# Kernel tuning notes

Measured on AMD Instinct MI355X. Metric: run time of the kernel, lower is better.

Reference implementation:

```python
import jax, jax.numpy as jnp
import numpy as np

G, N, D, K, OUT = 2048, 64, 128, 128, 10  # K*D == input_dim == 16384

def setup_inputs() -> dict:
    key = jax.random.key(0)
    k1, k2, k3, k4, k5 = jax.random.split(key, 5)
    x = jax.random.normal(k1, (G, N, D), dtype=jnp.float32)
    # nn.Linear(node_dim, input_dim/node_dim): weight [K, D], bias [K]
    W_att = jax.random.normal(k2, (K, D), dtype=jnp.float32) * (1.0 / np.sqrt(D))
    b_att = jax.random.normal(k3, (K,), dtype=jnp.float32) * 0.01
    # nn.Linear(input_dim, output_dim): weight [OUT, K*D], bias [OUT]
    W1 = jax.random.normal(k4, (OUT, K * D), dtype=jnp.float32) * (1.0 / np.sqrt(K * D))
    b1 = jax.random.normal(k5, (OUT,), dtype=jnp.float32) * 0.01
    return {"x": x, "W_att": W_att, "b_att": b_att, "W1": W1, "b1": b1}

def reference(x, W_att, b_att, W1, b1):
    # Per-graph gram matrix X^T X : [G, D, D], quantized to 2 decimals
    gram = jnp.einsum('gnd,gne->gde', x, x)
    gram = jnp.round(gram * 100.0) / 100.0
    # attend: Linear(D -> K) applied row-wise to gram -> attn_coef [G, D, K]
    attn = jnp.einsum('gde,ke->gdk', gram, W_att) + b_att
    # attn_weights = attn^T ([G, K, D]); pooled = attn_weights @ gram -> [G, K, D]
    pooled = jnp.einsum('gdk,gde->gke', attn, gram)
    flat = pooled.reshape(x.shape[0], K * D)  # view(input_dim)
    # linear1 (dropout omitted: eval mode)
    return flat @ W1.T + b1
```

## Files before the change

### kernel.cpp

```cpp
#include <hip/hip_runtime.h>

typedef __attribute__((ext_vector_type(8)))  __bf16 bf16x8;
typedef __attribute__((ext_vector_type(4)))  __bf16 bf16x4;
typedef __attribute__((ext_vector_type(16))) float  f32x16;

constexpr int NG  = 2048;
constexpr int NN  = 64;
constexpr int DD  = 128;
constexpr int KK  = 128;
constexpr int OUTD = 10;

__device__ __host__ inline void tileOf(int t, int& ti, int& tj) {
    if (t < 4)      { ti = 0; tj = t;     }
    else if (t < 7) { ti = 1; tj = t - 3; }
    else if (t < 9) { ti = 2; tj = t - 5; }
    else            { ti = 3; tj = 3;     }
}

__device__ inline int xtIdx(int r, int c) { return r * 64  + (c ^ ((r & 7) << 3)); }
__device__ inline int gIdx (int r, int c) { return r * 128 + (c ^ ((r & 15) << 3)); }

__global__ __launch_bounds__(128)
void precompute_kernel(const float* __restrict__ Wa,
                       const float* __restrict__ b_att,
                       const float* __restrict__ W1,
                       float* __restrict__ A,
                       float* __restrict__ c)
{
    const int o = blockIdx.x >> 7;
    const int f = blockIdx.x & 127;
    const int e = threadIdx.x;
    const float* __restrict__ W1o = W1 + (size_t)o * (KK * DD);

    float acc = 0.f, cacc = 0.f;
    for (int k = 0; k < KK; ++k) {
        const float w1 = W1o[k * DD + e];
        acc  += Wa[k * DD + f] * w1;
        cacc += b_att[k] * w1;
    }
    A[((size_t)o * DD + f) * DD + e] = acc;
    if (f == 0) c[o * DD + e] = cacc;
}

__global__ __launch_bounds__(256)
void pack_kernel(const float* __restrict__ A, __bf16* __restrict__ Sp)
{
    const int b = blockIdx.x;
    const int o = b / 10, t = b - o * 10;
    int ti, tj; tileOf(t, ti, tj);
    const int l  = threadIdx.x & 63;
    const int rq = threadIdx.x >> 6;
    const int e  = tj * 32 + (l & 31);
    const float* __restrict__ Ao = A + (size_t)o * DD * DD;

    bf16x4 p;
#pragma unroll
    for (int j = 0; j < 4; ++j) {
        const int f = ti * 32 + j + 8 * rq + 4 * (l >> 5);
        float v;
        if (f < e)       v = Ao[f * DD + e] + Ao[e * DD + f];
        else if (f == e) v = Ao[f * DD + f];
        else             v = 0.f;
        p[j] = (__bf16)v;
    }
    *(bf16x4*)&Sp[(size_t)((o * 10 + t) * 64 + l) * 16 + rq * 4] = p;
}

__device__ __forceinline__ void process_graph(
    const float* __restrict__ xg,
    __bf16* __restrict__ XtL, __bf16* __restrict__ GL,
    float (*__restrict__ sp)[DD], float* __restrict__ sOut,
    int tid, int w, int l, int l31, int l5, int extraBase,
    f32x16& hacc0, f32x16& haccX)
{
    {
        const int f = tid & 127, half = tid >> 7;
#pragma unroll
        for (int ch = 0; ch < 2; ++ch) {
            float v[8];
#pragma unroll
            for (int i = 0; i < 8; ++i) v[i] = xg[(half * 16 + ch * 8 + i) * DD + f];
            bf16x8 p;
#pragma unroll
            for (int i = 0; i < 8; ++i) p[i] = (__bf16)v[i];
            *(bf16x8*)&XtL[xtIdx(f, half * 16 + ch * 8)] = p;
        }
    }
    __syncthreads();

    const int ti  = w & 3;
    const int tj0 = (w >> 2) * 2;
    f32x16 acc0, acc1;
#pragma unroll
    for (int i = 0; i < 16; ++i) { acc0[i] = 0.f; acc1[i] = 0.f; }
    {
        const int arow  = ti  * 32 + l31;
        const int brow0 = tj0 * 32 + l31;
#pragma unroll
        for (int ks = 0; ks < 4; ++ks) {
            const int kc = ks * 16 + l5 * 8;
            bf16x8 a  = *(const bf16x8*)&XtL[xtIdx(arow, kc)];
            bf16x8 b0 = *(const bf16x8*)&XtL[xtIdx(brow0, kc)];
            bf16x8 b1 = *(const bf16x8*)&XtL[xtIdx(brow0 + 32, kc)];
            acc0 = __builtin_amdgcn_mfma_f32_32x32x16_bf16(a, b0, acc0, 0, 0, 0);
            acc1 = __builtin_amdgcn_mfma_f32_32x32x16_bf16(a, b1, acc1, 0, 0, 0);
        }
    }
    __syncthreads();

    {
        float sum0 = 0.f, sum1 = 0.f;
#pragma unroll
        for (int tt = 0; tt < 2; ++tt) {
            const int e = (tj0 + tt) * 32 + l31;
#pragma unroll
            for (int g2 = 0; g2 < 4; ++g2) {
                bf16x4 p;
#pragma unroll
                for (int j = 0; j < 4; ++j) {
                    const float av = tt ? acc1[g2 * 4 + j] : acc0[g2 * 4 + j];
                    const float q = rintf(av * 100.f) * 0.01f;
                    p[j] = (__bf16)q;
                    if (tt) sum1 += q; else sum0 += q;
                }
                const int fbase = ti * 32 + g2 * 8 + l5 * 4;
                *(bf16x4*)&GL[gIdx(e, fbase)] = p;
            }
        }
        sp[ti * 2 + l5][tj0 * 32 + l31]       = sum0;
        sp[ti * 2 + l5][(tj0 + 1) * 32 + l31] = sum1;
    }
    __syncthreads();

    if (w == 2 || w == 3) {
        const int e = (w - 2) * 64 + l;
        float s = 0.f;
#pragma unroll
        for (int i = 0; i < 8; ++i) s += sp[i][e];
        sOut[e] = s;
    }

#pragma unroll
    for (int i = 0; i < 16; ++i) hacc0[i] = 0.f;
    {
        int hti, htj; tileOf(w, hti, htj);
        const int ra = hti * 32 + l31, rb = htj * 32 + l31;
#pragma unroll
        for (int ks = 0; ks < 8; ++ks) {
            const int kc = ks * 16 + l5 * 8;
            bf16x8 a = *(const bf16x8*)&GL[gIdx(ra, kc)];
            bf16x8 b = *(const bf16x8*)&GL[gIdx(rb, kc)];
            hacc0 = __builtin_amdgcn_mfma_f32_32x32x16_bf16(a, b, hacc0, 0, 0, 0);
        }
    }
    if (w == extraBase || w == extraBase + 1) {
        int ti1, tj1; tileOf(8 + (w - extraBase), ti1, tj1);
        const int ra = ti1 * 32 + l31, rb = tj1 * 32 + l31;
#pragma unroll
        for (int ks = 0; ks < 8; ++ks) {
            const int kc = ks * 16 + l5 * 8;
            bf16x8 a = *(const bf16x8*)&GL[gIdx(ra, kc)];
            bf16x8 b = *(const bf16x8*)&GL[gIdx(rb, kc)];
            haccX = __builtin_amdgcn_mfma_f32_32x32x16_bf16(a, b, haccX, 0, 0, 0);
        }
    }
    __syncthreads();
}

__global__ __launch_bounds__(512)
void graph_kernel(const float* __restrict__ x,
                  const __bf16* __restrict__ Sp,
                  const float* __restrict__ cg,
                  const float* __restrict__ bias1,
                  float* __restrict__ out)
{
    __shared__ __align__(16) char ldsraw[20 * 512 * 4];
    __shared__ float sp[8][DD];
    __shared__ float sA[DD], sB[DD];

    __bf16* const XtL = (__bf16*)ldsraw;
    __bf16* const GL  = (__bf16*)ldsraw;
    float*  const PP  = (float*)ldsraw;

    const int g0  = blockIdx.x * 2;
    const int g1  = g0 + 1;
    const int tid = threadIdx.x;
    const int w   = tid >> 6;
    const int l   = tid & 63;
    const int l31 = l & 31;
    const int l5  = l >> 5;

    f32x16 hA0, hB0, hX1;
#pragma unroll
    for (int i = 0; i < 16; ++i) hX1[i] = 0.f;

    process_graph(x + (size_t)g0 * NN * DD, XtL, GL, sp, sA,
                  tid, w, l, l31, l5, 6, hA0, hX1);
    process_graph(x + (size_t)g1 * NN * DD, XtL, GL, sp, sB,
                  tid, w, l, l31, l5, 4, hB0, hX1);

#pragma unroll
    for (int o = 0; o < OUTD; ++o) {
        const __bf16* __restrict__ spp = Sp + (size_t)((o * 10 + w) * 64 + l) * 16;
        const bf16x8 s0 = *(const bf16x8*)&spp[0];
        const bf16x8 s1 = *(const bf16x8*)&spp[8];
        float tA = 0.f, tB = 0.f;
#pragma unroll
        for (int j = 0; j < 8; ++j) {
            const float v = (float)s0[j];
            tA += v * hA0[j];
            tB += v * hB0[j];
        }
#pragma unroll
        for (int j = 0; j < 8; ++j) {
            const float v = (float)s1[j];
            tA += v * hA0[8 + j];
            tB += v * hB0[8 + j];
        }
        if (w >= 4) {
            const __bf16* __restrict__ sp2 =
                Sp + (size_t)((o * 10 + 8 + (w & 1)) * 64 + l) * 16;
            const bf16x8 e0 = *(const bf16x8*)&sp2[0];
            const bf16x8 e1 = *(const bf16x8*)&sp2[8];
            float tx = 0.f;
#pragma unroll
            for (int j = 0; j < 8; ++j) tx += (float)e0[j] * hX1[j];
#pragma unroll
            for (int j = 0; j < 8; ++j) tx += (float)e1[j] * hX1[8 + j];
            if (w >= 6) tA += tx; else tB += tx;
        }
        if (w == 0) {
            tA += cg[o * DD + l] * sA[l] + cg[o * DD + 64 + l] * sA[64 + l];
            tB += cg[o * DD + l] * sB[l] + cg[o * DD + 64 + l] * sB[64 + l];
        }
        PP[o * 512 + tid]        = tA;
        PP[(10 + o) * 512 + tid] = tB;
    }
    __syncthreads();

    for (int p = w; p < 2 * OUTD; p += 8) {
        const float4 q0 = *(const float4*)&PP[p * 512 + l * 8];
        const float4 q1 = *(const float4*)&PP[p * 512 + l * 8 + 4];
        float v = (q0.x + q0.y) + (q0.z + q0.w) + (q1.x + q1.y) + (q1.z + q1.w);
        v += __shfl_down(v, 32, 64);
        v += __shfl_down(v, 16, 64);
        v += __shfl_down(v, 8, 64);
        v += __shfl_down(v, 4, 64);
        v += __shfl_down(v, 2, 64);
        v += __shfl_down(v, 1, 64);
        if (l == 0) {
            const int gg = (p < OUTD) ? g0 : g1;
            const int oo = (p < OUTD) ? p : p - OUTD;
            out[(size_t)gg * OUTD + oo] = v + bias1[oo];
        }
    }
}

extern "C" void kernel_launch(void* const* d_in, const int* in_sizes, int n_in,
                              void* d_out, int out_size, void* d_ws, size_t ws_size,
                              hipStream_t stream)
{
    const float* x     = (const float*)d_in[0];
    const float* Wa    = (const float*)d_in[1];
    const float* b_att = (const float*)d_in[2];
    const float* W1    = (const float*)d_in[3];
    const float* bias1 = (const float*)d_in[4];
    float* out = (float*)d_out;

    float*  A  = (float*)d_ws;
    float*  c  = A + (size_t)OUTD * DD * DD;
    __bf16* Sp = (__bf16*)(c + OUTD * DD);

    precompute_kernel<<<OUTD * DD, 128, 0, stream>>>(Wa, b_att, W1, A, c);
    pack_kernel<<<100, 256, 0, stream>>>(A, Sp);
    graph_kernel<<<NG / 2, 512, 0, stream>>>(x, Sp, c, bias1, out);
}
```

Measured before the change: 51.30 us.

## Prefetch second graph's input during first graph's gram MFMA phase

Before the first graph's gram MFMA loop, the kernel now issues the global loads for the second graph. After that loop it converts them to bf16 and stores them into a new dedicated LDS buffer, so the second graph's load latency overlaps with the first graph's compute. The first graph's staging moves into the kernel body, and the second graph's separate staging phase and its barrier are removed. The cost is 16 extra live float registers and an extra 16 KB of LDS, which may reduce occupancy.

```diff
diff --git a/kernel.cpp b/kernel.cpp
--- a/kernel.cpp
+++ b/kernel.cpp
@@ -66,27 +66,22 @@
     *(bf16x4*)&Sp[(size_t)((o * 10 + t) * 64 + l) * 16 + rq * 4] = p;
 }
 
-__device__ __forceinline__ void process_graph(
-    const float* __restrict__ xg,
-    __bf16* __restrict__ XtL, __bf16* __restrict__ GL,
+template<bool PREP_B>
+__device__ __forceinline__ void phases123(
+    const float* __restrict__ xgB,
+    const __bf16* __restrict__ XtS,
+    __bf16* __restrict__ XtLB,
+    __bf16* __restrict__ GL,
     float (*__restrict__ sp)[DD], float* __restrict__ sOut,
     int tid, int w, int l, int l31, int l5, int extraBase,
     f32x16& hacc0, f32x16& haccX)
 {
-    {
+    float vB[16];
+    if (PREP_B) {
         const int f = tid & 127, half = tid >> 7;
 #pragma unroll
-        for (int ch = 0; ch < 2; ++ch) {
-            float v[8];
-#pragma unroll
-            for (int i = 0; i < 8; ++i) v[i] = xg[(half * 16 + ch * 8 + i) * DD + f];
-            bf16x8 p;
-#pragma unroll
-            for (int i = 0; i < 8; ++i) p[i] = (__bf16)v[i];
-            *(bf16x8*)&XtL[xtIdx(f, half * 16 + ch * 8)] = p;
-        }
-    }
-    __syncthreads();
+        for (int i = 0; i < 16; ++i) vB[i] = xgB[(half * 16 + i) * DD + f];
+    }
 
     const int ti  = w & 3;
     const int tj0 = (w >> 2) * 2;
@@ -99,12 +94,21 @@
 #pragma unroll
         for (int ks = 0; ks < 4; ++ks) {
             const int kc = ks * 16 + l5 * 8;
-            bf16x8 a  = *(const bf16x8*)&XtL[xtIdx(arow, kc)];
-            bf16x8 b0 = *(const bf16x8*)&XtL[xtIdx(brow0, kc)];
-            bf16x8 b1 = *(const bf16x8*)&XtL[xtIdx(brow0 + 32, kc)];
+            bf16x8 a  = *(const bf16x8*)&XtS[xtIdx(arow, kc)];
+            bf16x8 b0 = *(const bf16x8*)&XtS[xtIdx(brow0, kc)];
+            bf16x8 b1 = *(const bf16x8*)&XtS[xtIdx(brow0 + 32, kc)];
             acc0 = __builtin_amdgcn_mfma_f32_32x32x16_bf16(a, b0, acc0, 0, 0, 0);
             acc1 = __builtin_amdgcn_mfma_f32_32x32x16_bf16(a, b1, acc1, 0, 0, 0);
         }
+    }
+
+    if (PREP_B) {
+        const int f = tid & 127, half = tid >> 7;
+        bf16x8 p0, p1;
+#pragma unroll
+        for (int i = 0; i < 8; ++i) { p0[i] = (__bf16)vB[i]; p1[i] = (__bf16)vB[8 + i]; }
+        *(bf16x8*)&XtLB[xtIdx(f, half * 16)]     = p0;
+        *(bf16x8*)&XtLB[xtIdx(f, half * 16 + 8)] = p1;
     }
     __syncthreads();
 
@@ -175,12 +179,13 @@
                   float* __restrict__ out)
 {
     __shared__ __align__(16) char ldsraw[20 * 512 * 4];
+    __shared__ __align__(16) __bf16 XtLB[DD * NN];
     __shared__ float sp[8][DD];
     __shared__ float sA[DD], sB[DD];
 
-    __bf16* const XtL = (__bf16*)ldsraw;
-    __bf16* const GL  = (__bf16*)ldsraw;
-    float*  const PP  = (float*)ldsraw;
+    __bf16* const XtLA = (__bf16*)ldsraw;
+    __bf16* const GL   = (__bf16*)ldsraw;
+    float*  const PP   = (float*)ldsraw;
 
     const int g0  = blockIdx.x * 2;
     const int g1  = g0 + 1;
@@ -189,15 +194,32 @@
     const int l   = tid & 63;
     const int l31 = l & 31;
     const int l5  = l >> 5;
+    const float* __restrict__ xgA = x + (size_t)g0 * NN * DD;
+    const float* __restrict__ xgB = x + (size_t)g1 * NN * DD;
+
+    {
+        const int f = tid & 127, half = tid >> 7;
+#pragma unroll
+        for (int ch = 0; ch < 2; ++ch) {
+            float v[8];
+#pragma unroll
+            for (int i = 0; i < 8; ++i) v[i] = xgA[(half * 16 + ch * 8 + i) * DD + f];
+            bf16x8 p;
+#pragma unroll
+            for (int i = 0; i < 8; ++i) p[i] = (__bf16)v[i];
+            *(bf16x8*)&XtLA[xtIdx(f, half * 16 + ch * 8)] = p;
+        }
+    }
+    __syncthreads();
 
     f32x16 hA0, hB0, hX1;
 #pragma unroll
     for (int i = 0; i < 16; ++i) hX1[i] = 0.f;
 
-    process_graph(x + (size_t)g0 * NN * DD, XtL, GL, sp, sA,
-                  tid, w, l, l31, l5, 6, hA0, hX1);
-    process_graph(x + (size_t)g1 * NN * DD, XtL, GL, sp, sB,
-                  tid, w, l, l31, l5, 4, hB0, hX1);
+    phases123<true>(xgB, XtLA, XtLB, GL, sp, sA,
+                    tid, w, l, l31, l5, 6, hA0, hX1);
+    phases123<false>(nullptr, XtLB, nullptr, GL, sp, sB,
+                     tid, w, l, l31, l5, 4, hB0, hX1);
 
 #pragma unroll
     for (int o = 0; o < OUTD; ++o) {
```

After: 51.83 us. No clear change (+1.0%).

## Split LDS into separate Xt and gram buffers and prefetch second graph's input

Applied to the files above, without the earlier changes.

Inlines the two per-graph passes and gives the transposed-input and gram tiles separate LDS regions, so the second graph's x is loaded into registers and written to LDS while the first graph's gram-gram MFMAs run. This removes one barrier per graph and hides global load latency behind compute. It also sets launch bounds to request two blocks per CU, and batches the final projection loop two outputs at a time with the cg values hoisted. The risks are higher register pressure from holding 16 prefetched floats plus the accumulators, and a larger LDS footprint (48 KB) that may limit occupancy.

```diff
diff --git a/kernel.cpp b/kernel.cpp
--- a/kernel.cpp
+++ b/kernel.cpp
@@ -66,121 +66,20 @@
     *(bf16x4*)&Sp[(size_t)((o * 10 + t) * 64 + l) * 16 + rq * 4] = p;
 }
 
-__device__ __forceinline__ void process_graph(
-    const float* __restrict__ xg,
-    __bf16* __restrict__ XtL, __bf16* __restrict__ GL,
-    float (*__restrict__ sp)[DD], float* __restrict__ sOut,
-    int tid, int w, int l, int l31, int l5, int extraBase,
-    f32x16& hacc0, f32x16& haccX)
-{
-    {
-        const int f = tid & 127, half = tid >> 7;
-#pragma unroll
-        for (int ch = 0; ch < 2; ++ch) {
-            float v[8];
-#pragma unroll
-            for (int i = 0; i < 8; ++i) v[i] = xg[(half * 16 + ch * 8 + i) * DD + f];
-            bf16x8 p;
-#pragma unroll
-            for (int i = 0; i < 8; ++i) p[i] = (__bf16)v[i];
-            *(bf16x8*)&XtL[xtIdx(f, half * 16 + ch * 8)] = p;
-        }
-    }
-    __syncthreads();
-
-    const int ti  = w & 3;
-    const int tj0 = (w >> 2) * 2;
-    f32x16 acc0, acc1;
-#pragma unroll
-    for (int i = 0; i < 16; ++i) { acc0[i] = 0.f; acc1[i] = 0.f; }
-    {
-        const int arow  = ti  * 32 + l31;
-        const int brow0 = tj0 * 32 + l31;
-#pragma unroll
-        for (int ks = 0; ks < 4; ++ks) {
-            const int kc = ks * 16 + l5 * 8;
-            bf16x8 a  = *(const bf16x8*)&XtL[xtIdx(arow, kc)];
-            bf16x8 b0 = *(const bf16x8*)&XtL[xtIdx(brow0, kc)];
-            bf16x8 b1 = *(const bf16x8*)&XtL[xtIdx(brow0 + 32, kc)];
-            acc0 = __builtin_amdgcn_mfma_f32_32x32x16_bf16(a, b0, acc0, 0, 0, 0);
-            acc1 = __builtin_amdgcn_mfma_f32_32x32x16_bf16(a, b1, acc1, 0, 0, 0);
-        }
-    }
-    __syncthreads();
-
-    {
-        float sum0 = 0.f, sum1 = 0.f;
-#pragma unroll
-        for (int tt = 0; tt < 2; ++tt) {
-            const int e = (tj0 + tt) * 32 + l31;
-#pragma unroll
-            for (int g2 = 0; g2 < 4; ++g2) {
-                bf16x4 p;
-#pragma unroll
-                for (int j = 0; j < 4; ++j) {
-                    const float av = tt ? acc1[g2 * 4 + j] : acc0[g2 * 4 + j];
-                    const float q = rintf(av * 100.f) * 0.01f;
-                    p[j] = (__bf16)q;
-                    if (tt) sum1 += q; else sum0 += q;
-                }
-                const int fbase = ti * 32 + g2 * 8 + l5 * 4;
-                *(bf16x4*)&GL[gIdx(e, fbase)] = p;
-            }
-        }
-        sp[ti * 2 + l5][tj0 * 32 + l31]       = sum0;
-        sp[ti * 2 + l5][(tj0 + 1) * 32 + l31] = sum1;
-    }
-    __syncthreads();
-
-    if (w == 2 || w == 3) {
-        const int e = (w - 2) * 64 + l;
-        float s = 0.f;
-#pragma unroll
-        for (int i = 0; i < 8; ++i) s += sp[i][e];
-        sOut[e] = s;
-    }
-
-#pragma unroll
-    for (int i = 0; i < 16; ++i) hacc0[i] = 0.f;
-    {
-        int hti, htj; tileOf(w, hti, htj);
-        const int ra = hti * 32 + l31, rb = htj * 32 + l31;
-#pragma unroll
-        for (int ks = 0; ks < 8; ++ks) {
-            const int kc = ks * 16 + l5 * 8;
-            bf16x8 a = *(const bf16x8*)&GL[gIdx(ra, kc)];
-            bf16x8 b = *(const bf16x8*)&GL[gIdx(rb, kc)];
-            hacc0 = __builtin_amdgcn_mfma_f32_32x32x16_bf16(a, b, hacc0, 0, 0, 0);
-        }
-    }
-    if (w == extraBase || w == extraBase + 1) {
-        int ti1, tj1; tileOf(8 + (w - extraBase), ti1, tj1);
-        const int ra = ti1 * 32 + l31, rb = tj1 * 32 + l31;
-#pragma unroll
-        for (int ks = 0; ks < 8; ++ks) {
-            const int kc = ks * 16 + l5 * 8;
-            bf16x8 a = *(const bf16x8*)&GL[gIdx(ra, kc)];
-            bf16x8 b = *(const bf16x8*)&GL[gIdx(rb, kc)];
-            haccX = __builtin_amdgcn_mfma_f32_32x32x16_bf16(a, b, haccX, 0, 0, 0);
-        }
-    }
-    __syncthreads();
-}
-
-__global__ __launch_bounds__(512)
+__global__ __launch_bounds__(512, 2)
 void graph_kernel(const float* __restrict__ x,
                   const __bf16* __restrict__ Sp,
                   const float* __restrict__ cg,
                   const float* __restrict__ bias1,
                   float* __restrict__ out)
 {
-    __shared__ __align__(16) char ldsraw[20 * 512 * 4];
+    __shared__ __align__(16) char lds48[48 * 1024];
     __shared__ float sp[8][DD];
     __shared__ float sA[DD], sB[DD];
 
-    __bf16* const XtL = (__bf16*)ldsraw;
-    __bf16* const GL  = (__bf16*)ldsraw;
-    float*  const PP  = (float*)ldsraw;
+    __bf16* const XtL = (__bf16*)lds48;
+    __bf16* const GL  = (__bf16*)(lds48 + 16 * 1024);
+    float*  const PP  = (float*)lds48;
 
     const int g0  = blockIdx.x * 2;
     const int g1  = g0 + 1;
@@ -189,52 +88,253 @@
     const int l   = tid & 63;
     const int l31 = l & 31;
     const int l5  = l >> 5;
+    const int f   = tid & 127, half = tid >> 7;
+    const float* __restrict__ xgA = x + (size_t)g0 * NN * DD;
+    const float* __restrict__ xgB = x + (size_t)g1 * NN * DD;
+
+    const int ti  = w & 3;
+    const int tj0 = (w >> 2) * 2;
+
+    {
+#pragma unroll
+        for (int ch = 0; ch < 2; ++ch) {
+            float v[8];
+#pragma unroll
+            for (int i = 0; i < 8; ++i) v[i] = xgA[(half * 16 + ch * 8 + i) * DD + f];
+            bf16x8 p;
+#pragma unroll
+            for (int i = 0; i < 8; ++i) p[i] = (__bf16)v[i];
+            *(bf16x8*)&XtL[xtIdx(f, half * 16 + ch * 8)] = p;
+        }
+    }
+    __syncthreads();
 
     f32x16 hA0, hB0, hX1;
 #pragma unroll
     for (int i = 0; i < 16; ++i) hX1[i] = 0.f;
 
-    process_graph(x + (size_t)g0 * NN * DD, XtL, GL, sp, sA,
-                  tid, w, l, l31, l5, 6, hA0, hX1);
-    process_graph(x + (size_t)g1 * NN * DD, XtL, GL, sp, sB,
-                  tid, w, l, l31, l5, 4, hB0, hX1);
-
-#pragma unroll
-    for (int o = 0; o < OUTD; ++o) {
-        const __bf16* __restrict__ spp = Sp + (size_t)((o * 10 + w) * 64 + l) * 16;
-        const bf16x8 s0 = *(const bf16x8*)&spp[0];
-        const bf16x8 s1 = *(const bf16x8*)&spp[8];
-        float tA = 0.f, tB = 0.f;
-#pragma unroll
-        for (int j = 0; j < 8; ++j) {
-            const float v = (float)s0[j];
-            tA += v * hA0[j];
-            tB += v * hB0[j];
-        }
-#pragma unroll
-        for (int j = 0; j < 8; ++j) {
-            const float v = (float)s1[j];
-            tA += v * hA0[8 + j];
-            tB += v * hB0[8 + j];
-        }
-        if (w >= 4) {
-            const __bf16* __restrict__ sp2 =
-                Sp + (size_t)((o * 10 + 8 + (w & 1)) * 64 + l) * 16;
-            const bf16x8 e0 = *(const bf16x8*)&sp2[0];
-            const bf16x8 e1 = *(const bf16x8*)&sp2[8];
-            float tx = 0.f;
-#pragma unroll
-            for (int j = 0; j < 8; ++j) tx += (float)e0[j] * hX1[j];
-#pragma unroll
-            for (int j = 0; j < 8; ++j) tx += (float)e1[j] * hX1[8 + j];
-            if (w >= 6) tA += tx; else tB += tx;
-        }
+    f32x16 acc0, acc1;
+#pragma unroll
+    for (int i = 0; i < 16; ++i) { acc0[i] = 0.f; acc1[i] = 0.f; }
+    {
+        const int arow  = ti  * 32 + l31;
+        const int brow0 = tj0 * 32 + l31;
+#pragma unroll
+        for (int ks = 0; ks < 4; ++ks) {
+            const int kc = ks * 16 + l5 * 8;
+            bf16x8 a  = *(const bf16x8*)&XtL[xtIdx(arow, kc)];
+            bf16x8 b0 = *(const bf16x8*)&XtL[xtIdx(brow0, kc)];
+            bf16x8 b1 = *(const bf16x8*)&XtL[xtIdx(brow0 + 32, kc)];
+            acc0 = __builtin_amdgcn_mfma_f32_32x32x16_bf16(a, b0, acc0, 0, 0, 0);
+            acc1 = __builtin_amdgcn_mfma_f32_32x32x16_bf16(a, b1, acc1, 0, 0, 0);
+        }
+    }
+    {
+        float sum0 = 0.f, sum1 = 0.f;
+#pragma unroll
+        for (int tt = 0; tt < 2; ++tt) {
+            const int e = (tj0 + tt) * 32 + l31;
+#pragma unroll
+            for (int g2 = 0; g2 < 4; ++g2) {
+                bf16x4 p;
+#pragma unroll
+                for (int j = 0; j < 4; ++j) {
+                    const float av = tt ? acc1[g2 * 4 + j] : acc0[g2 * 4 + j];
+                    const float q = rintf(av * 100.f) * 0.01f;
+                    p[j] = (__bf16)q;
+                    if (tt) sum1 += q; else sum0 += q;
+                }
+                *(bf16x4*)&GL[gIdx(e, ti * 32 + g2 * 8 + l5 * 4)] = p;
+            }
+        }
+        sp[ti * 2 + l5][tj0 * 32 + l31]       = sum0;
+        sp[ti * 2 + l5][(tj0 + 1) * 32 + l31] = sum1;
+    }
+    __syncthreads();
+
+    float vB[16];
+#pragma unroll
+    for (int i = 0; i < 16; ++i) vB[i] = xgB[(half * 16 + i) * DD + f];
+
+    if (w == 2 || w == 3) {
+        const int e = (w - 2) * 64 + l;
+        float s = 0.f;
+#pragma unroll
+        for (int i = 0; i < 8; ++i) s += sp[i][e];
+        sA[e] = s;
+    }
+
+#pragma unroll
+    for (int i = 0; i < 16; ++i) hA0[i] = 0.f;
+    {
+        int hti, htj; tileOf(w, hti, htj);
+        const int ra = hti * 32 + l31, rb = htj * 32 + l31;
+#pragma unroll
+        for (int ks = 0; ks < 8; ++ks) {
+            const int kc = ks * 16 + l5 * 8;
+            bf16x8 a = *(const bf16x8*)&GL[gIdx(ra, kc)];
+            bf16x8 b = *(const bf16x8*)&GL[gIdx(rb, kc)];
+            hA0 = __builtin_amdgcn_mfma_f32_32x32x16_bf16(a, b, hA0, 0, 0, 0);
+        }
+    }
+    if (w >= 6) {
+        int ti1, tj1; tileOf(8 + (w - 6), ti1, tj1);
+        const int ra = ti1 * 32 + l31, rb = tj1 * 32 + l31;
+#pragma unroll
+        for (int ks = 0; ks < 8; ++ks) {
+            const int kc = ks * 16 + l5 * 8;
+            bf16x8 a = *(const bf16x8*)&GL[gIdx(ra, kc)];
+            bf16x8 b = *(const bf16x8*)&GL[gIdx(rb, kc)];
+            hX1 = __builtin_amdgcn_mfma_f32_32x32x16_bf16(a, b, hX1, 0, 0, 0);
+        }
+    }
+    {
+        bf16x8 p0, p1;
+#pragma unroll
+        for (int i = 0; i < 8; ++i) { p0[i] = (__bf16)vB[i]; p1[i] = (__bf16)vB[8 + i]; }
+        *(bf16x8*)&XtL[xtIdx(f, half * 16)]     = p0;
+        *(bf16x8*)&XtL[xtIdx(f, half * 16 + 8)] = p1;
+    }
+    __syncthreads();
+
+#pragma unroll
+    for (int i = 0; i < 16; ++i) { acc0[i] = 0.f; acc1[i] = 0.f; }
+    {
+        const int arow  = ti  * 32 + l31;
+        const int brow0 = tj0 * 32 + l31;
+#pragma unroll
+        for (int ks = 0; ks < 4; ++ks) {
+            const int kc = ks * 16 + l5 * 8;
+            bf16x8 a  = *(const bf16x8*)&XtL[xtIdx(arow, kc)];
+            bf16x8 b0 = *(const bf16x8*)&XtL[xtIdx(brow0, kc)];
+            bf16x8 b1 = *(const bf16x8*)&XtL[xtIdx(brow0 + 32, kc)];
+            acc0 = __builtin_amdgcn_mfma_f32_32x32x16_bf16(a, b0, acc0, 0, 0, 0);
+            acc1 = __builtin_amdgcn_mfma_f32_32x32x16_bf16(a, b1, acc1, 0, 0, 0);
+        }
+    }
+    {
+        float sum0 = 0.f, sum1 = 0.f;
+#pragma unroll
+        for (int tt = 0; tt < 2; ++tt) {
+            const int e = (tj0 + tt) * 32 + l31;
+#pragma unroll
+            for (int g2 = 0; g2 < 4; ++g2) {
+                bf16x4 p;
+#pragma unroll
+                for (int j = 0; j < 4; ++j) {
+                    const float av = tt ? acc1[g2 * 4 + j] : acc0[g2 * 4 + j];
+                    const float q = rintf(av * 100.f) * 0.01f;
+                    p[j] = (__bf16)q;
+                    if (tt) sum1 += q; else sum0 += q;
+                }
+                *(bf16x4*)&GL[gIdx(e, ti * 32 + g2 * 8 + l5 * 4)] = p;
+            }
+        }
+        sp[ti * 2 + l5][tj0 * 32 + l31]       = sum0;
+        sp[ti * 2 + l5][(tj0 + 1) * 32 + l31] = sum1;
+    }
+    __syncthreads();
+
+    if (w == 2 || w == 3) {
+        const int e = (w - 2) * 64 + l;
+        float s = 0.f;
+#pragma unroll
+        for (int i = 0; i < 8; ++i) s += sp[i][e];
+        sB[e] = s;
+    }
+#pragma unroll
+    for (int i = 0; i < 16; ++i) hB0[i] = 0.f;
+    {
+        int hti, htj; tileOf(w, hti, htj);
+        const int ra = hti * 32 + l31, rb = htj * 32 + l31;
+#pragma unroll
+        for (int ks = 0; ks < 8; ++ks) {
+            const int kc = ks * 16 + l5 * 8;
+            bf16x8 a = *(const bf16x8*)&GL[gIdx(ra, kc)];
+            bf16x8 b = *(const bf16x8*)&GL[gIdx(rb, kc)];
+            hB0 = __builtin_amdgcn_mfma_f32_32x32x16_bf16(a, b, hB0, 0, 0, 0);
+        }
+    }
+    if (w == 4 || w == 5) {
+        int ti1, tj1; tileOf(8 + (w - 4), ti1, tj1);
+        const int ra = ti1 * 32 + l31, rb = tj1 * 32 + l31;
+#pragma unroll
+        for (int ks = 0; ks < 8; ++ks) {
+            const int kc = ks * 16 + l5 * 8;
+            bf16x8 a = *(const bf16x8*)&GL[gIdx(ra, kc)];
+            bf16x8 b = *(const bf16x8*)&GL[gIdx(rb, kc)];
+            hX1 = __builtin_amdgcn_mfma_f32_32x32x16_bf16(a, b, hX1, 0, 0, 0);
+        }
+    }
+    __syncthreads();
+
+    {
+        float cgv[2 * OUTD];
         if (w == 0) {
-            tA += cg[o * DD + l] * sA[l] + cg[o * DD + 64 + l] * sA[64 + l];
-            tB += cg[o * DD + l] * sB[l] + cg[o * DD + 64 + l] * sB[64 + l];
-        }
-        PP[o * 512 + tid]        = tA;
-        PP[(10 + o) * 512 + tid] = tB;
+#pragma unroll
+            for (int o = 0; o < OUTD; ++o) {
+                cgv[2 * o]     = cg[o * DD + l];
+                cgv[2 * o + 1] = cg[o * DD + 64 + l];
+            }
+        }
+        const __bf16* __restrict__ SpM = Sp + (size_t)(w * 64 + l) * 16;
+        const __bf16* __restrict__ SpX = Sp + (size_t)((8 + (w & 1)) * 64 + l) * 16;
+        const float sAl = sA[l], sAh = sA[64 + l];
+        const float sBl = sB[l], sBh = sB[64 + l];
+
+#pragma unroll
+        for (int ob = 0; ob < 5; ++ob) {
+            const int o0 = 2 * ob, o1 = 2 * ob + 1;
+            const bf16x8 m0a = *(const bf16x8*)&SpM[(size_t)o0 * 10240];
+            const bf16x8 m0b = *(const bf16x8*)&SpM[(size_t)o0 * 10240 + 8];
+            const bf16x8 m1a = *(const bf16x8*)&SpM[(size_t)o1 * 10240];
+            const bf16x8 m1b = *(const bf16x8*)&SpM[(size_t)o1 * 10240 + 8];
+            bf16x8 x0a, x0b, x1a, x1b;
+            if (w >= 4) {
+                x0a = *(const bf16x8*)&SpX[(size_t)o0 * 10240];
+                x0b = *(const bf16x8*)&SpX[(size_t)o0 * 10240 + 8];
+                x1a = *(const bf16x8*)&SpX[(size_t)o1 * 10240];
+                x1b = *(const bf16x8*)&SpX[(size_t)o1 * 10240 + 8];
+            }
+            float tA0 = 0.f, tB0 = 0.f, tA1 = 0.f, tB1 = 0.f;
+#pragma unroll
+            for (int j = 0; j < 8; ++j) {
+                const float v0 = (float)m0a[j], v1 = (float)m1a[j];
+                tA0 += v0 * hA0[j];      tB0 += v0 * hB0[j];
+                tA1 += v1 * hA0[j];      tB1 += v1 * hB0[j];
+            }
+#pragma unroll
+            for (int j = 0; j < 8; ++j) {
+                const float v0 = (float)m0b[j], v1 = (float)m1b[j];
+                tA0 += v0 * hA0[8 + j];  tB0 += v0 * hB0[8 + j];
+                tA1 += v1 * hA0[8 + j];  tB1 += v1 * hB0[8 + j];
+            }
+            if (w >= 4) {
+                float tx0 = 0.f, tx1 = 0.f;
+#pragma unroll
+                for (int j = 0; j < 8; ++j) {
+                    tx0 += (float)x0a[j] * hX1[j];
+                    tx1 += (float)x1a[j] * hX1[j];
+                }
+#pragma unroll
+                for (int j = 0; j < 8; ++j) {
+                    tx0 += (float)x0b[j] * hX1[8 + j];
+                    tx1 += (float)x1b[j] * hX1[8 + j];
+                }
+                if (w >= 6) { tA0 += tx0; tA1 += tx1; }
+                else        { tB0 += tx0; tB1 += tx1; }
+            }
+            if (w == 0) {
+                tA0 += cgv[2 * o0] * sAl + cgv[2 * o0 + 1] * sAh;
+                tB0 += cgv[2 * o0] * sBl + cgv[2 * o0 + 1] * sBh;
+                tA1 += cgv[2 * o1] * sAl + cgv[2 * o1 + 1] * sAh;
+                tB1 += cgv[2 * o1] * sBl + cgv[2 * o1 + 1] * sBh;
+            }
+            PP[o0 * 512 + tid]        = tA0;
+            PP[(10 + o0) * 512 + tid] = tB0;
+            PP[o1 * 512 + tid]        = tA1;
+            PP[(10 + o1) * 512 + tid] = tB1;
+        }
     }
     __syncthreads();
 
```

New measurement: 58.51 us. +14.1%, slower.
